# Optimization experiments

Hardware: AMD Instinct MI355X
Metric: run time of the kernel (lower is better)

## Reference

```python
import jax, jax.numpy as jnp
import numpy as np

SEQ_LEN, INPUT_DIM, HIDDEN_DIM, NUM_CLASSES, BATCH = 512, 256, 1024, 128, 256


def setup_inputs() -> dict:
    key = jax.random.key(0)
    ks = jax.random.split(key, 12)
    sx = np.sqrt(2.0 / INPUT_DIM).astype(np.float32)
    sh = np.sqrt(2.0 / HIDDEN_DIM).astype(np.float32)
    inp = {
        "x": jax.random.randint(ks[0], (BATCH, SEQ_LEN, 1), 0, NUM_CLASSES, dtype=jnp.int32),
        "emb": jax.random.normal(ks[1], (NUM_CLASSES, INPUT_DIM), jnp.float32),
        "Wcx": jax.random.normal(ks[2], (HIDDEN_DIM, INPUT_DIM), jnp.float32) * sx,
        "bc": jnp.zeros((HIDDEN_DIM,), jnp.float32),
        "Wix": jax.random.normal(ks[3], (HIDDEN_DIM, INPUT_DIM), jnp.float32) * sx,
        "Wih": jax.random.normal(ks[4], (HIDDEN_DIM, HIDDEN_DIM), jnp.float32) * sh,
        "bi": jnp.zeros((HIDDEN_DIM,), jnp.float32),
        "Wfx": jax.random.normal(ks[5], (HIDDEN_DIM, INPUT_DIM), jnp.float32) * sx,
        "Wfh": jax.random.normal(ks[6], (HIDDEN_DIM, HIDDEN_DIM), jnp.float32) * sh,
        "bf": jnp.zeros((HIDDEN_DIM,), jnp.float32),
        "Wox": jax.random.normal(ks[7], (HIDDEN_DIM, INPUT_DIM), jnp.float32) * sx,
        "Woh": jax.random.normal(ks[8], (HIDDEN_DIM, HIDDEN_DIM), jnp.float32) * sh,
        "bo": jnp.zeros((HIDDEN_DIM,), jnp.float32),
        "Wph": jax.random.normal(ks[9], (NUM_CLASSES, HIDDEN_DIM), jnp.float32) * sh,
        "bp": jnp.zeros((NUM_CLASSES,), jnp.float32),
    }
    return inp


def reference(x, emb, Wcx, bc, Wix, Wih, bi, Wfx, Wfh, bf, Wox, Woh, bo, Wph, bp):
    B = x.shape[0]
    H = Wfh.shape[0]
    xt = emb[x[:, :, 0]]                       # [B, S, I] embedded inputs
    # Precompute the input-to-gate projections (parallel over time; identical math)
    xf = jnp.einsum("bsi,hi->sbh", xt, Wfx)    # [S, B, H]
    xi = jnp.einsum("bsi,hi->sbh", xt, Wix)
    xo = jnp.einsum("bsi,hi->sbh", xt, Wox)
    xc = jnp.einsum("bsi,hi->sbh", xt, Wcx)

    def step(carry, inputs):
        c, h = carry
        xf_t, xi_t, xo_t, xc_t = inputs
        # peephole gates read cell state c, not h
        f = jax.nn.sigmoid(xf_t + c @ Wfh.T + bf)
        i = jax.nn.sigmoid(xi_t + c @ Wih.T + bi)
        o = jax.nn.sigmoid(xo_t + c @ Woh.T + bo)
        c_new = jax.nn.sigmoid(xc_t + bc) * i + c * f
        h_new = jnp.tanh(c_new) * o
        return (c_new, h_new), None

    c0 = jnp.zeros((B, H), xt.dtype)
    h0 = jnp.zeros((B, H), xt.dtype)
    (c_T, h_T), _ = jax.lax.scan(step, (c0, h0), (xf, xi, xo, xc))
    p = h_T @ Wph.T + bp                       # [B, num_classes]
    return jax.nn.log_softmax(p, axis=1)
```

## Files before the change

kernel.cpp:

```cpp
#include <hip/hip_runtime.h>

#define SEQ  512
#define IDIM 256
#define H    1024
#define NC   128
#define B    256
#define NBLK 256

typedef __attribute__((ext_vector_type(8))) short bh8;
typedef __attribute__((ext_vector_type(4))) float f4;
typedef __attribute__((ext_vector_type(4))) int i4;

__device__ __forceinline__ float sigf(float x) { return 1.0f / (1.0f + __expf(-x)); }

__device__ __forceinline__ unsigned short bf16r(float v) {
    unsigned u = __builtin_bit_cast(unsigned, v);
    u += 0x7fffu + ((u >> 16) & 1u);
    return (unsigned short)(u >> 16);
}

__global__ __launch_bounds__(256) void tables_kernel(
    const float* __restrict__ emb,
    const float* __restrict__ Wcx, const float* __restrict__ bc,
    const float* __restrict__ Wix, const float* __restrict__ bi,
    const float* __restrict__ Wfx, const float* __restrict__ bf,
    const float* __restrict__ Wox, const float* __restrict__ bo,
    float* __restrict__ FF, float* __restrict__ II,
    float* __restrict__ OO, float* __restrict__ G)
{
    const int k = blockIdx.x;
    const int h = blockIdx.y * 256 + threadIdx.x;
    __shared__ float e[IDIM];
    e[threadIdx.x] = emb[k * IDIM + threadIdx.x];
    __syncthreads();
    const float4* e4  = (const float4*)e;
    const float4* wf4 = (const float4*)(Wfx + (size_t)h * IDIM);
    const float4* wi4 = (const float4*)(Wix + (size_t)h * IDIM);
    const float4* wo4 = (const float4*)(Wox + (size_t)h * IDIM);
    const float4* wc4 = (const float4*)(Wcx + (size_t)h * IDIM);
    float aF = 0.f, aI = 0.f, aO = 0.f, aC = 0.f;
#pragma unroll 4
    for (int i = 0; i < IDIM / 4; i++) {
        float4 ev = e4[i];
        float4 a = wf4[i]; aF += ev.x * a.x + ev.y * a.y + ev.z * a.z + ev.w * a.w;
        float4 b = wi4[i]; aI += ev.x * b.x + ev.y * b.y + ev.z * b.z + ev.w * b.w;
        float4 c = wo4[i]; aO += ev.x * c.x + ev.y * c.y + ev.z * c.z + ev.w * c.w;
        float4 d = wc4[i]; aC += ev.x * d.x + ev.y * d.y + ev.z * d.z + ev.w * d.w;
    }
    const int o = k * H + h;
    FF[o] = aF + bf[h];
    II[o] = aI + bi[h];
    OO[o] = aO + bo[h];
    G[o]  = sigf(aC + bc[h]);
}

__global__ __launch_bounds__(256) void swz_kernel(const float* __restrict__ W,
                                                  unsigned short* __restrict__ D)
{
    int g = blockIdx.x * 256 + threadIdx.x;
    int h  = g >> 7;
    int kc = (g & 127) << 3;
    const float4* s = (const float4*)(W + (size_t)h * H + kc);
    float4 a = s[0], b = s[1];
    unsigned short tmp[8] = { bf16r(a.x), bf16r(a.y), bf16r(a.z), bf16r(a.w),
                              bf16r(b.x), bf16r(b.y), bf16r(b.z), bf16r(b.w) };
    int nb = h >> 4, kb = kc >> 5, quad = (kc >> 3) & 3;
    int lane = (h & 15) + (quad << 4);
    bh8 v;
#pragma unroll
    for (int j = 0; j < 8; j++) v[j] = (short)tmp[j];
    *(bh8*)(D + (size_t)((nb * 32 + kb) * 512 + lane * 8)) = v;
}

__global__ __launch_bounds__(256, 1) void persist_kernel(
    const unsigned short* __restrict__ Wf, const unsigned short* __restrict__ Wi,
    const unsigned short* __restrict__ Wo,
    const float* __restrict__ FF, const float* __restrict__ II,
    const float* __restrict__ OO, const float* __restrict__ G,
    const int* __restrict__ x,
    unsigned short* c16a, unsigned short* c16b,
    float* __restrict__ hb, int* flags)
{
    const int blk = blockIdx.x;
    const int rt = blk >> 4;
    const int nt = blk & 15;
    const int tid  = threadIdx.x;
    const int wave = tid >> 6;
    const int lane = tid & 63;
    const int l15 = lane & 15, quad = lane >> 4;

    __shared__ unsigned short cs[16 * 1024];

    const int row0 = rt * 16;
    const int abase = l15 * 1024;
    const int asw = l15 & 7;
    const int hcol = nt * 64 + wave * 16 + l15;
    const int nb = nt * 4 + wave;

    const unsigned short* wfp = Wf + (size_t)nb * 32 * 512 + (size_t)lane * 8;
    const unsigned short* wip = Wi + (size_t)nb * 32 * 512 + (size_t)lane * 8;
    const unsigned short* wop = Wo + (size_t)nb * 32 * 512 + (size_t)lane * 8;

    bh8 wf_r[32], wi_r[32];
#pragma unroll
    for (int kt = 0; kt < 32; kt++) {
        wf_r[kt] = *(const bh8*)(wfp + (size_t)kt * 512);
        wi_r[kt] = *(const bh8*)(wip + (size_t)kt * 512);
    }

    float cn_keep[4] = {0.f, 0.f, 0.f, 0.f};
    int* const myflag = flags + rt * 64 + nt * 4 + wave;
    const int* const pf = flags + rt * 64 + lane;

    for (int s = 0; s < SEQ; s++) {
        const unsigned short* cur16 = (s & 1) ? c16b : c16a;
        unsigned short*       nxt16 = (s & 1) ? c16a : c16b;

        float ffv[4], iiv[4], ggv[4];
#pragma unroll
        for (int r = 0; r < 4; r++) {
            int b = row0 + quad * 4 + r;
            int tok = x[b * SEQ + s];
            ffv[r] = FF[tok * H + hcol];
            iiv[r] = II[tok * H + hcol];
            ggv[r] = G[tok * H + hcol];
        }

        f4 accF = {0.f, 0.f, 0.f, 0.f}, accI = {0.f, 0.f, 0.f, 0.f};
        if (s > 0) {
            {
                int guard = 0;
                for (;;) {
                    int fv;
                    asm volatile("global_load_dword %0, %1, off sc0 sc1\n\ts_waitcnt vmcnt(0)"
                                 : "=v"(fv) : "v"(pf) : "memory");
                    if (__all(fv >= s)) break;
                    if (++guard > (1 << 20)) break;
                }
            }
            i4 tmp[8];
#pragma unroll
            for (int i = 0; i < 8; i++) {
                int chunk = i * 256 + tid;
                int row = chunk >> 7, g = chunk & 127;
                const i4* p = (const i4*)(cur16 + (size_t)(row0 + row) * H + g * 8);
                asm volatile("global_load_dwordx4 %0, %1, off sc0 sc1"
                             : "=v"(tmp[i]) : "v"(p));
            }
            asm volatile("s_waitcnt vmcnt(0)" ::: "memory");
#pragma unroll
            for (int i = 0; i < 8; i++) {
                int chunk = i * 256 + tid;
                int row = chunk >> 7, g = chunk & 127;
                *(i4*)(cs + row * 1024 + ((g ^ (row & 7)) << 3)) = tmp[i];
            }
            __syncthreads();
#pragma unroll
            for (int kt = 0; kt < 32; kt++) {
                bh8 a = *(const bh8*)(cs + abase + (((kt * 4 + quad) ^ asw) << 3));
                accF = __builtin_amdgcn_mfma_f32_16x16x32_bf16(a, wf_r[kt], accF, 0, 0, 0);
                accI = __builtin_amdgcn_mfma_f32_16x16x32_bf16(a, wi_r[kt], accI, 0, 0, 0);
            }
        }

#pragma unroll
        for (int r = 0; r < 4; r++) {
            float f = sigf(ffv[r] + accF[r]);
            float i = sigf(iiv[r] + accI[r]);
            float cn = ggv[r] * i + cn_keep[r] * f;
            cn_keep[r] = cn;
            int b = row0 + quad * 4 + r;
            unsigned us = bf16r(cn);
            unsigned ot = (unsigned)__shfl_xor((int)us, 1);
            if (s < SEQ - 1 && (lane & 1) == 0) {
                unsigned dw = us | (ot << 16);
                unsigned* p = (unsigned*)(nxt16 + (size_t)b * H + hcol);
                asm volatile("global_atomic_swap %0, %1, off sc1"
                             :: "v"(p), "v"(dw) : "memory");
            }
        }

        if (s < SEQ - 1) {
            asm volatile("s_waitcnt vmcnt(0)" ::: "memory");
            if (lane == 0) {
                int v = s + 1;
                asm volatile("global_atomic_swap %0, %1, off sc1"
                             :: "v"(myflag), "v"(v) : "memory");
            }
        }
    }

    f4 accO = {0.f, 0.f, 0.f, 0.f};
#pragma unroll 4
    for (int kt = 0; kt < 32; kt++) {
        bh8 a  = *(const bh8*)(cs + abase + (((kt * 4 + quad) ^ asw) << 3));
        bh8 bo = *(const bh8*)(wop + (size_t)kt * 512);
        accO = __builtin_amdgcn_mfma_f32_16x16x32_bf16(a, bo, accO, 0, 0, 0);
    }
#pragma unroll
    for (int r = 0; r < 4; r++) {
        int b = row0 + quad * 4 + r;
        int tok = x[b * SEQ + (SEQ - 1)];
        float o = sigf(OO[tok * H + hcol] + accO[r]);
        hb[(size_t)b * H + hcol] = tanhf(cn_keep[r]) * o;
    }
}

__global__ __launch_bounds__(128) void out_kernel(
    const float* __restrict__ hbuf, const float* __restrict__ Wph,
    const float* __restrict__ bp, float* __restrict__ out)
{
    const int b = blockIdx.x;
    const int j = threadIdx.x;
    __shared__ float hs[H];
    for (int t = j; t < H; t += 128) hs[t] = hbuf[(size_t)b * H + t];
    __syncthreads();
    const float4* w4 = (const float4*)(Wph + (size_t)j * H);
    const float4* h4 = (const float4*)hs;
    float acc = bp[j];
#pragma unroll 4
    for (int k = 0; k < H / 4; k++) {
        float4 a = w4[k], v = h4[k];
        acc += a.x * v.x + a.y * v.y + a.z * v.z + a.w * v.w;
    }
    __shared__ float red[128];
    red[j] = acc; __syncthreads();
    for (int off = 64; off > 0; off >>= 1) { if (j < off) red[j] = fmaxf(red[j], red[j + off]); __syncthreads(); }
    float m = red[0]; __syncthreads();
    red[j] = __expf(acc - m); __syncthreads();
    for (int off = 64; off > 0; off >>= 1) { if (j < off) red[j] += red[j + off]; __syncthreads(); }
    float lse = m + __logf(red[0]);
    out[(size_t)b * NC + j] = acc - lse;
}

extern "C" void kernel_launch(void* const* d_in, const int* in_sizes, int n_in,
                              void* d_out, int out_size, void* d_ws, size_t ws_size,
                              hipStream_t stream)
{
    const int*   x   = (const int*)d_in[0];
    const float* emb = (const float*)d_in[1];
    const float* Wcx = (const float*)d_in[2];
    const float* bc  = (const float*)d_in[3];
    const float* Wix = (const float*)d_in[4];
    const float* Wih = (const float*)d_in[5];
    const float* bi  = (const float*)d_in[6];
    const float* Wfx = (const float*)d_in[7];
    const float* Wfh = (const float*)d_in[8];
    const float* bf  = (const float*)d_in[9];
    const float* Wox = (const float*)d_in[10];
    const float* Woh = (const float*)d_in[11];
    const float* bo  = (const float*)d_in[12];
    const float* Wph = (const float*)d_in[13];
    const float* bp  = (const float*)d_in[14];
    float* out = (float*)d_out;

    char* wsb = (char*)d_ws;
    float* FF = (float*)(wsb + 0);
    float* II = (float*)(wsb + (512 << 10));
    float* OO = (float*)(wsb + (1024 << 10));
    float* G  = (float*)(wsb + (1536 << 10));
    float* hb = (float*)(wsb + (2048 << 10));
    int*   flags = (int*)(wsb + (3072 << 10));
    unsigned short* Wf_sw = (unsigned short*)(wsb + (4096 << 10));
    unsigned short* Wi_sw = (unsigned short*)(wsb + (6144 << 10));
    unsigned short* Wo_sw = (unsigned short*)(wsb + (8192 << 10));
    unsigned short* c16a  = (unsigned short*)(wsb + (10240 << 10));
    unsigned short* c16b  = (unsigned short*)(wsb + (10752 << 10));

    hipMemsetAsync(flags, 0, 4096, stream);

    tables_kernel<<<dim3(NC, 4), 256, 0, stream>>>(emb, Wcx, bc, Wix, bi, Wfx, bf, Wox, bo,
                                                   FF, II, OO, G);
    swz_kernel<<<512, 256, 0, stream>>>(Wfh, Wf_sw);
    swz_kernel<<<512, 256, 0, stream>>>(Wih, Wi_sw);
    swz_kernel<<<512, 256, 0, stream>>>(Woh, Wo_sw);

    persist_kernel<<<NBLK, 256, 0, stream>>>(Wf_sw, Wi_sw, Wo_sw, FF, II, OO, G, x,
                                             c16a, c16b, hb, flags);

    out_kernel<<<B, 128, 0, stream>>>(hb, Wph, bp, out);
}
```

Before: 2.340 ms.

## Replace per-wave flag barrier with step-tagged cell-state words for dataflow sync

Each cell-state element is now stored as a 32-bit word whose high half carries the step tag and low half the bf16 value. Consumers poll the data itself until every tag reaches the current step, re-polling only the chunks that are not yet ready. This removes the separate flag write, the vmcnt wait before it, and the flag-polling round trip, so data and readiness arrive together. The cost is that cell-state traffic and global loads double, and readers must unpack the tagged words with perm instructions.

```diff
diff --git a/kernel.cpp b/kernel.cpp
--- a/kernel.cpp
+++ b/kernel.cpp
@@ -18,6 +18,8 @@
     u += 0x7fffu + ((u >> 16) & 1u);
     return (unsigned short)(u >> 16);
 }
+
+__device__ __forceinline__ unsigned umin2(unsigned a, unsigned b) { return a < b ? a : b; }
 
 __global__ __launch_bounds__(256) void tables_kernel(
     const float* __restrict__ emb,
@@ -78,8 +80,8 @@
     const float* __restrict__ FF, const float* __restrict__ II,
     const float* __restrict__ OO, const float* __restrict__ G,
     const int* __restrict__ x,
-    unsigned short* c16a, unsigned short* c16b,
-    float* __restrict__ hb, int* flags)
+    unsigned* c32a, unsigned* c32b,
+    float* __restrict__ hb)
 {
     const int blk = blockIdx.x;
     const int rt = blk >> 4;
@@ -109,12 +111,10 @@
     }
 
     float cn_keep[4] = {0.f, 0.f, 0.f, 0.f};
-    int* const myflag = flags + rt * 64 + nt * 4 + wave;
-    const int* const pf = flags + rt * 64 + lane;
 
     for (int s = 0; s < SEQ; s++) {
-        const unsigned short* cur16 = (s & 1) ? c16b : c16a;
-        unsigned short*       nxt16 = (s & 1) ? c16a : c16b;
+        const unsigned* curb = (s & 1) ? c32b : c32a;
+        unsigned*       nxtb = (s & 1) ? c32a : c32b;
 
         float ffv[4], iiv[4], ggv[4];
 #pragma unroll
@@ -128,31 +128,52 @@
 
         f4 accF = {0.f, 0.f, 0.f, 0.f}, accI = {0.f, 0.f, 0.f, 0.f};
         if (s > 0) {
-            {
-                int guard = 0;
-                for (;;) {
-                    int fv;
-                    asm volatile("global_load_dword %0, %1, off sc0 sc1\n\ts_waitcnt vmcnt(0)"
-                                 : "=v"(fv) : "v"(pf) : "memory");
-                    if (__all(fv >= s)) break;
-                    if (++guard > (1 << 20)) break;
+            const unsigned thrs = ((unsigned)s) << 16;
+            i4 ta[8], tb[8];
+            bool done[8];
+#pragma unroll
+            for (int i = 0; i < 8; i++) done[i] = false;
+            int guard = 0;
+            for (;;) {
+#pragma unroll
+                for (int i = 0; i < 8; i++) {
+                    if (!done[i]) {
+                        int chunk = i * 256 + tid;
+                        int row = chunk >> 7, g = chunk & 127;
+                        const i4* p = (const i4*)(curb + (size_t)(row0 + row) * 1024 + g * 8);
+                        asm volatile("global_load_dwordx4 %0, %1, off sc0 sc1"
+                                     : "=v"(ta[i]) : "v"(p));
+                        asm volatile("global_load_dwordx4 %0, %1, off sc0 sc1"
+                                     : "=v"(tb[i]) : "v"(p + 1));
+                    }
                 }
-            }
-            i4 tmp[8];
+                asm volatile("s_waitcnt vmcnt(0)" ::: "memory");
+                bool all = true;
+#pragma unroll
+                for (int i = 0; i < 8; i++) {
+                    if (!done[i]) {
+                        unsigned m = umin2(
+                            umin2(umin2((unsigned)ta[i].x, (unsigned)ta[i].y),
+                                  umin2((unsigned)ta[i].z, (unsigned)ta[i].w)),
+                            umin2(umin2((unsigned)tb[i].x, (unsigned)tb[i].y),
+                                  umin2((unsigned)tb[i].z, (unsigned)tb[i].w)));
+                        done[i] = (m >= thrs);
+                    }
+                    all = all && done[i];
+                }
+                if (all) break;
+                if (++guard > (1 << 16)) break;
+            }
 #pragma unroll
             for (int i = 0; i < 8; i++) {
                 int chunk = i * 256 + tid;
                 int row = chunk >> 7, g = chunk & 127;
-                const i4* p = (const i4*)(cur16 + (size_t)(row0 + row) * H + g * 8);
-                asm volatile("global_load_dwordx4 %0, %1, off sc0 sc1"
-                             : "=v"(tmp[i]) : "v"(p));
-            }
-            asm volatile("s_waitcnt vmcnt(0)" ::: "memory");
-#pragma unroll
-            for (int i = 0; i < 8; i++) {
-                int chunk = i * 256 + tid;
-                int row = chunk >> 7, g = chunk & 127;
-                *(i4*)(cs + row * 1024 + ((g ^ (row & 7)) << 3)) = tmp[i];
+                i4 pv;
+                pv.x = (int)__builtin_amdgcn_perm((unsigned)ta[i].y, (unsigned)ta[i].x, 0x05040100u);
+                pv.y = (int)__builtin_amdgcn_perm((unsigned)ta[i].w, (unsigned)ta[i].z, 0x05040100u);
+                pv.z = (int)__builtin_amdgcn_perm((unsigned)tb[i].y, (unsigned)tb[i].x, 0x05040100u);
+                pv.w = (int)__builtin_amdgcn_perm((unsigned)tb[i].w, (unsigned)tb[i].z, 0x05040100u);
+                *(i4*)(cs + row * 1024 + ((g ^ (row & 7)) << 3)) = pv;
             }
             __syncthreads();
 #pragma unroll
@@ -163,29 +184,19 @@
             }
         }
 
+        const unsigned tagw = ((unsigned)(s + 1)) << 16;
 #pragma unroll
         for (int r = 0; r < 4; r++) {
             float f = sigf(ffv[r] + accF[r]);
             float i = sigf(iiv[r] + accI[r]);
             float cn = ggv[r] * i + cn_keep[r] * f;
             cn_keep[r] = cn;
-            int b = row0 + quad * 4 + r;
-            unsigned us = bf16r(cn);
-            unsigned ot = (unsigned)__shfl_xor((int)us, 1);
-            if (s < SEQ - 1 && (lane & 1) == 0) {
-                unsigned dw = us | (ot << 16);
-                unsigned* p = (unsigned*)(nxt16 + (size_t)b * H + hcol);
+            if (s < SEQ - 1) {
+                int b = row0 + quad * 4 + r;
+                unsigned dw = tagw | (unsigned)bf16r(cn);
+                unsigned* p = nxtb + (size_t)b * 1024 + hcol;
                 asm volatile("global_atomic_swap %0, %1, off sc1"
                              :: "v"(p), "v"(dw) : "memory");
-            }
-        }
-
-        if (s < SEQ - 1) {
-            asm volatile("s_waitcnt vmcnt(0)" ::: "memory");
-            if (lane == 0) {
-                int v = s + 1;
-                asm volatile("global_atomic_swap %0, %1, off sc1"
-                             :: "v"(myflag), "v"(v) : "memory");
             }
         }
     }
@@ -260,14 +271,13 @@
     float* OO = (float*)(wsb + (1024 << 10));
     float* G  = (float*)(wsb + (1536 << 10));
     float* hb = (float*)(wsb + (2048 << 10));
-    int*   flags = (int*)(wsb + (3072 << 10));
-    unsigned short* Wf_sw = (unsigned short*)(wsb + (4096 << 10));
-    unsigned short* Wi_sw = (unsigned short*)(wsb + (6144 << 10));
-    unsigned short* Wo_sw = (unsigned short*)(wsb + (8192 << 10));
-    unsigned short* c16a  = (unsigned short*)(wsb + (10240 << 10));
-    unsigned short* c16b  = (unsigned short*)(wsb + (10752 << 10));
-
-    hipMemsetAsync(flags, 0, 4096, stream);
+    unsigned* c32a = (unsigned*)(wsb + (3072 << 10));
+    unsigned* c32b = (unsigned*)(wsb + (4096 << 10));
+    unsigned short* Wf_sw = (unsigned short*)(wsb + (5120 << 10));
+    unsigned short* Wi_sw = (unsigned short*)(wsb + (7168 << 10));
+    unsigned short* Wo_sw = (unsigned short*)(wsb + (9216 << 10));
+
+    hipMemsetAsync(c32a, 0, 2 << 20, stream);
 
     tables_kernel<<<dim3(NC, 4), 256, 0, stream>>>(emb, Wcx, bc, Wix, bi, Wfx, bf, Wox, bo,
                                                    FF, II, OO, G);
@@ -276,7 +286,7 @@
     swz_kernel<<<512, 256, 0, stream>>>(Woh, Wo_sw);
 
     persist_kernel<<<NBLK, 256, 0, stream>>>(Wf_sw, Wi_sw, Wo_sw, FF, II, OO, G, x,
-                                             c16a, c16b, hb, flags);
+                                             c32a, c32b, hb);
 
     out_kernel<<<B, 128, 0, stream>>>(hb, Wph, bp, out);
 }
```

After: 3.090 ms. +32.0%, slower.

## Ping-pong two batch row groups per block to overlap sync latency with compute

Applied to the files above, without the earlier changes.

Halves the persistent grid so each block handles two 16-row batch groups (A and B) that share the same register-resident weight tiles. The step loop is software-pipelined: while group A's flag poll and global loads of the previous cell state are in flight, the epilogue and flag publish for group B run, and the reverse. The aim is to hide the cross-block flag-wait and global-load latency of the recurrence behind useful work. In exchange each block does twice the MFMA and epilogue work per step, uses twice the LDS, and only half as many CUs participate.

```diff
diff --git a/kernel.cpp b/kernel.cpp
--- a/kernel.cpp
+++ b/kernel.cpp
@@ -5,7 +5,7 @@
 #define H    1024
 #define NC   128
 #define B    256
-#define NBLK 256
+#define NBLK 128
 
 typedef __attribute__((ext_vector_type(8))) short bh8;
 typedef __attribute__((ext_vector_type(4))) float f4;
@@ -72,6 +72,56 @@
     *(bh8*)(D + (size_t)((nb * 32 + kb) * 512 + lane * 8)) = v;
 }
 
+#define ATOMSW(p_, v_) asm volatile("global_atomic_swap %0, %1, off sc1" :: "v"(p_), "v"(v_) : "memory")
+#define POLL(pf_, thr_)                                                                     \
+    { int guard_ = 0;                                                                       \
+      for (;;) { int fv_;                                                                   \
+        asm volatile("global_load_dword %0, %1, off sc0 sc1\n\ts_waitcnt vmcnt(0)"          \
+                     : "=v"(fv_) : "v"(pf_) : "memory");                                    \
+        if (__all(fv_ >= (thr_))) break;                                                    \
+        if (++guard_ > (1 << 20)) break; } }
+#define STAGE_ISSUE(tmp_, cur_, row0_)                                                      \
+    _Pragma("unroll")                                                                       \
+    for (int i_ = 0; i_ < 8; i_++) {                                                        \
+        int chunk_ = i_ * 256 + tid;                                                        \
+        int row_ = chunk_ >> 7, g_ = chunk_ & 127;                                          \
+        const i4* p_ = (const i4*)((cur_) + (size_t)((row0_) + row_) * H + g_ * 8);         \
+        asm volatile("global_load_dwordx4 %0, %1, off sc0 sc1" : "=v"(tmp_[i_]) : "v"(p_)); }
+#define LDS_WRITE(cs_, tmp_)                                                                \
+    _Pragma("unroll")                                                                       \
+    for (int i_ = 0; i_ < 8; i_++) {                                                        \
+        int chunk_ = i_ * 256 + tid;                                                        \
+        int row_ = chunk_ >> 7, g_ = chunk_ & 127;                                          \
+        *(i4*)((cs_) + row_ * 1024 + ((g_ ^ (row_ & 7)) << 3)) = tmp_[i_]; }
+#define LOAD_TABLES(row0_, s_, ffv_, iiv_, ggv_)                                            \
+    _Pragma("unroll")                                                                       \
+    for (int r_ = 0; r_ < 4; r_++) {                                                        \
+        int b_ = (row0_) + quad * 4 + r_;                                                   \
+        int tok_ = x[b_ * SEQ + (s_)];                                                      \
+        ffv_[r_] = FF[tok_ * H + hcol];                                                     \
+        iiv_[r_] = II[tok_ * H + hcol];                                                     \
+        ggv_[r_] = G[tok_ * H + hcol]; }
+#define MFMA32(cs_, accF_, accI_)                                                           \
+    _Pragma("unroll")                                                                       \
+    for (int kt_ = 0; kt_ < 32; kt_++) {                                                    \
+        bh8 a_ = *(const bh8*)((cs_) + abase + (((kt_ * 4 + quad) ^ asw) << 3));            \
+        accF_ = __builtin_amdgcn_mfma_f32_16x16x32_bf16(a_, wf_r[kt_], accF_, 0, 0, 0);     \
+        accI_ = __builtin_amdgcn_mfma_f32_16x16x32_bf16(a_, wi_r[kt_], accI_, 0, 0, 0); }
+#define EPILOGUE(ffv_, iiv_, ggv_, accF_, accI_, cn_, row0_, nxt_, do_store_)               \
+    _Pragma("unroll")                                                                       \
+    for (int r_ = 0; r_ < 4; r_++) {                                                        \
+        float f_ = sigf(ffv_[r_] + accF_[r_]);                                              \
+        float i_ = sigf(iiv_[r_] + accI_[r_]);                                              \
+        float cn2_ = ggv_[r_] * i_ + cn_[r_] * f_;                                          \
+        cn_[r_] = cn2_;                                                                     \
+        int b_ = (row0_) + quad * 4 + r_;                                                   \
+        unsigned us_ = bf16r(cn2_);                                                         \
+        unsigned ot_ = (unsigned)__shfl_xor((int)us_, 1);                                   \
+        if ((do_store_) && (lane & 1) == 0) {                                               \
+            unsigned dw_ = us_ | (ot_ << 16);                                               \
+            unsigned* p_ = (unsigned*)((nxt_) + (size_t)b_ * H + hcol);                     \
+            ATOMSW(p_, dw_); } }
+
 __global__ __launch_bounds__(256, 1) void persist_kernel(
     const unsigned short* __restrict__ Wf, const unsigned short* __restrict__ Wi,
     const unsigned short* __restrict__ Wo,
@@ -82,16 +132,18 @@
     float* __restrict__ hb, int* flags)
 {
     const int blk = blockIdx.x;
-    const int rt = blk >> 4;
-    const int nt = blk & 15;
+    const int set = blk >> 4;
+    const int nt  = blk & 15;
+    const int gA = set * 2, gB = set * 2 + 1;
+    const int rowA0 = gA * 16, rowB0 = gB * 16;
     const int tid  = threadIdx.x;
     const int wave = tid >> 6;
     const int lane = tid & 63;
     const int l15 = lane & 15, quad = lane >> 4;
 
-    __shared__ unsigned short cs[16 * 1024];
-
-    const int row0 = rt * 16;
+    __shared__ unsigned short csA[16 * 1024];
+    __shared__ unsigned short csB[16 * 1024];
+
     const int abase = l15 * 1024;
     const int asw = l15 & 7;
     const int hcol = nt * 64 + wave * 16 + l15;
@@ -108,101 +160,70 @@
         wi_r[kt] = *(const bh8*)(wip + (size_t)kt * 512);
     }
 
-    float cn_keep[4] = {0.f, 0.f, 0.f, 0.f};
-    int* const myflag = flags + rt * 64 + nt * 4 + wave;
-    const int* const pf = flags + rt * 64 + lane;
-
-    for (int s = 0; s < SEQ; s++) {
+    int* const mfA = flags + gA * 64 + nt * 4 + wave;
+    const int* const pfA = flags + gA * 64 + lane;
+    int* const mfB = flags + gB * 64 + nt * 4 + wave;
+    const int* const pfB = flags + gB * 64 + lane;
+
+    float cnA[4] = {0.f, 0.f, 0.f, 0.f}, cnB[4] = {0.f, 0.f, 0.f, 0.f};
+    f4 accFA = {0,0,0,0}, accIA = {0,0,0,0};
+    f4 accFB = {0,0,0,0}, accIB = {0,0,0,0};
+    float ffvA[4], iivA[4], ggvA[4], ffvB[4], iivB[4], ggvB[4];
+
+    LOAD_TABLES(rowA0, 0, ffvA, iivA, ggvA);
+    LOAD_TABLES(rowB0, 0, ffvB, iivB, ggvB);
+    EPILOGUE(ffvA, iivA, ggvA, accFA, accIA, cnA, rowA0, c16b, 1);
+    asm volatile("s_waitcnt vmcnt(0)" ::: "memory");
+    if (lane == 0) { int v = 1; ATOMSW(mfA, v); }
+
+    for (int s = 1; s < SEQ; s++) {
         const unsigned short* cur16 = (s & 1) ? c16b : c16a;
         unsigned short*       nxt16 = (s & 1) ? c16a : c16b;
-
-        float ffv[4], iiv[4], ggv[4];
-#pragma unroll
-        for (int r = 0; r < 4; r++) {
-            int b = row0 + quad * 4 + r;
-            int tok = x[b * SEQ + s];
-            ffv[r] = FF[tok * H + hcol];
-            iiv[r] = II[tok * H + hcol];
-            ggv[r] = G[tok * H + hcol];
-        }
-
-        f4 accF = {0.f, 0.f, 0.f, 0.f}, accI = {0.f, 0.f, 0.f, 0.f};
-        if (s > 0) {
-            {
-                int guard = 0;
-                for (;;) {
-                    int fv;
-                    asm volatile("global_load_dword %0, %1, off sc0 sc1\n\ts_waitcnt vmcnt(0)"
-                                 : "=v"(fv) : "v"(pf) : "memory");
-                    if (__all(fv >= s)) break;
-                    if (++guard > (1 << 20)) break;
-                }
-            }
-            i4 tmp[8];
-#pragma unroll
-            for (int i = 0; i < 8; i++) {
-                int chunk = i * 256 + tid;
-                int row = chunk >> 7, g = chunk & 127;
-                const i4* p = (const i4*)(cur16 + (size_t)(row0 + row) * H + g * 8);
-                asm volatile("global_load_dwordx4 %0, %1, off sc0 sc1"
-                             : "=v"(tmp[i]) : "v"(p));
-            }
-            asm volatile("s_waitcnt vmcnt(0)" ::: "memory");
-#pragma unroll
-            for (int i = 0; i < 8; i++) {
-                int chunk = i * 256 + tid;
-                int row = chunk >> 7, g = chunk & 127;
-                *(i4*)(cs + row * 1024 + ((g ^ (row & 7)) << 3)) = tmp[i];
-            }
-            __syncthreads();
-#pragma unroll
-            for (int kt = 0; kt < 32; kt++) {
-                bh8 a = *(const bh8*)(cs + abase + (((kt * 4 + quad) ^ asw) << 3));
-                accF = __builtin_amdgcn_mfma_f32_16x16x32_bf16(a, wf_r[kt], accF, 0, 0, 0);
-                accI = __builtin_amdgcn_mfma_f32_16x16x32_bf16(a, wi_r[kt], accI, 0, 0, 0);
-            }
-        }
-
-#pragma unroll
-        for (int r = 0; r < 4; r++) {
-            float f = sigf(ffv[r] + accF[r]);
-            float i = sigf(iiv[r] + accI[r]);
-            float cn = ggv[r] * i + cn_keep[r] * f;
-            cn_keep[r] = cn;
-            int b = row0 + quad * 4 + r;
-            unsigned us = bf16r(cn);
-            unsigned ot = (unsigned)__shfl_xor((int)us, 1);
-            if (s < SEQ - 1 && (lane & 1) == 0) {
-                unsigned dw = us | (ot << 16);
-                unsigned* p = (unsigned*)(nxt16 + (size_t)b * H + hcol);
-                asm volatile("global_atomic_swap %0, %1, off sc1"
-                             :: "v"(p), "v"(dw) : "memory");
-            }
-        }
-
-        if (s < SEQ - 1) {
-            asm volatile("s_waitcnt vmcnt(0)" ::: "memory");
-            if (lane == 0) {
-                int v = s + 1;
-                asm volatile("global_atomic_swap %0, %1, off sc1"
-                             :: "v"(myflag), "v"(v) : "memory");
-            }
-        }
-    }
-
-    f4 accO = {0.f, 0.f, 0.f, 0.f};
+        POLL(pfA, s);
+        i4 tmpA[8];
+        STAGE_ISSUE(tmpA, cur16, rowA0);
+        LOAD_TABLES(rowA0, s, ffvA, iivA, ggvA);
+        EPILOGUE(ffvB, iivB, ggvB, accFB, accIB, cnB, rowB0, cur16, 1);
+        asm volatile("s_waitcnt vmcnt(0)" ::: "memory");
+        if (lane == 0) { int v = s; ATOMSW(mfB, v); }
+        LDS_WRITE(csA, tmpA);
+        __syncthreads();
+        accFA = (f4){0,0,0,0}; accIA = (f4){0,0,0,0};
+        MFMA32(csA, accFA, accIA);
+        POLL(pfB, s);
+        i4 tmpB[8];
+        STAGE_ISSUE(tmpB, cur16, rowB0);
+        LOAD_TABLES(rowB0, s, ffvB, iivB, ggvB);
+        EPILOGUE(ffvA, iivA, ggvA, accFA, accIA, cnA, rowA0, nxt16, (s < SEQ - 1));
+        asm volatile("s_waitcnt vmcnt(0)" ::: "memory");
+        if (s < SEQ - 1 && lane == 0) { int v = s + 1; ATOMSW(mfA, v); }
+        LDS_WRITE(csB, tmpB);
+        __syncthreads();
+        accFB = (f4){0,0,0,0}; accIB = (f4){0,0,0,0};
+        MFMA32(csB, accFB, accIB);
+    }
+
+    EPILOGUE(ffvB, iivB, ggvB, accFB, accIB, cnB, rowB0, c16a, 0);
+
+    f4 accOA = {0,0,0,0}, accOB = {0,0,0,0};
 #pragma unroll 4
     for (int kt = 0; kt < 32; kt++) {
-        bh8 a  = *(const bh8*)(cs + abase + (((kt * 4 + quad) ^ asw) << 3));
         bh8 bo = *(const bh8*)(wop + (size_t)kt * 512);
-        accO = __builtin_amdgcn_mfma_f32_16x16x32_bf16(a, bo, accO, 0, 0, 0);
+        bh8 aA = *(const bh8*)(csA + abase + (((kt * 4 + quad) ^ asw) << 3));
+        bh8 aB = *(const bh8*)(csB + abase + (((kt * 4 + quad) ^ asw) << 3));
+        accOA = __builtin_amdgcn_mfma_f32_16x16x32_bf16(aA, bo, accOA, 0, 0, 0);
+        accOB = __builtin_amdgcn_mfma_f32_16x16x32_bf16(aB, bo, accOB, 0, 0, 0);
     }
 #pragma unroll
     for (int r = 0; r < 4; r++) {
-        int b = row0 + quad * 4 + r;
-        int tok = x[b * SEQ + (SEQ - 1)];
-        float o = sigf(OO[tok * H + hcol] + accO[r]);
-        hb[(size_t)b * H + hcol] = tanhf(cn_keep[r]) * o;
+        int bA = rowA0 + quad * 4 + r;
+        int tokA = x[bA * SEQ + (SEQ - 1)];
+        float oA = sigf(OO[tokA * H + hcol] + accOA[r]);
+        hb[(size_t)bA * H + hcol] = tanhf(cnA[r]) * oA;
+        int bB = rowB0 + quad * 4 + r;
+        int tokB = x[bB * SEQ + (SEQ - 1)];
+        float oB = sigf(OO[tokB * H + hcol] + accOB[r]);
+        hb[(size_t)bB * H + hcol] = tanhf(cnB[r]) * oB;
     }
 }
 
@@ -267,7 +288,7 @@
     unsigned short* c16a  = (unsigned short*)(wsb + (10240 << 10));
     unsigned short* c16b  = (unsigned short*)(wsb + (10752 << 10));
 
-    hipMemsetAsync(flags, 0, 4096, stream);
+    (void)hipMemsetAsync(flags, 0, 4096, stream);
 
     tables_kernel<<<dim3(NC, 4), 256, 0, stream>>>(emb, Wcx, bc, Wix, bi, Wfx, bf, Wox, bo,
                                                    FF, II, OO, G);
```

After: 5.595 ms. 2.39x slower.

## Use per-block flags and fetch ready producer slices eagerly in recurrent loop

Applied to the files above, without the earlier changes.

Replaces the per-wave readiness flags with one flag per block, published after a block-wide barrier. Consumers no longer wait until every producer is ready before loading. They ballot the flags and issue loads for each producer's 64-column slice as soon as that slice is ready, starting from the next neighbour to spread the traffic. Cell-state stores are widened to 64-bit atomic swaps. This overlaps loading with waiting and cuts flag traffic, at the cost of an extra __syncthreads per step and more, smaller loads.

```diff
diff --git a/kernel.cpp b/kernel.cpp
--- a/kernel.cpp
+++ b/kernel.cpp
@@ -10,6 +10,7 @@
 typedef __attribute__((ext_vector_type(8))) short bh8;
 typedef __attribute__((ext_vector_type(4))) float f4;
 typedef __attribute__((ext_vector_type(4))) int i4;
+typedef __attribute__((ext_vector_type(2))) int i2;
 
 __device__ __forceinline__ float sigf(float x) { return 1.0f / (1.0f + __expf(-x)); }
 
@@ -97,6 +98,9 @@
     const int hcol = nt * 64 + wave * 16 + l15;
     const int nb = nt * 4 + wave;
 
+    const int prow = tid >> 4;
+    const int pc8  = tid & 15;
+
     const unsigned short* wfp = Wf + (size_t)nb * 32 * 512 + (size_t)lane * 8;
     const unsigned short* wip = Wi + (size_t)nb * 32 * 512 + (size_t)lane * 8;
     const unsigned short* wop = Wo + (size_t)nb * 32 * 512 + (size_t)lane * 8;
@@ -109,8 +113,8 @@
     }
 
     float cn_keep[4] = {0.f, 0.f, 0.f, 0.f};
-    int* const myflag = flags + rt * 64 + nt * 4 + wave;
-    const int* const pf = flags + rt * 64 + lane;
+    int* const myflag = flags + rt * 16 + nt;
+    const int* const pf = flags + rt * 16 + (lane & 15);
 
     for (int s = 0; s < SEQ; s++) {
         const unsigned short* cur16 = (s & 1) ? c16b : c16a;
@@ -128,31 +132,33 @@
 
         f4 accF = {0.f, 0.f, 0.f, 0.f}, accI = {0.f, 0.f, 0.f, 0.f};
         if (s > 0) {
-            {
-                int guard = 0;
-                for (;;) {
-                    int fv;
-                    asm volatile("global_load_dword %0, %1, off sc0 sc1\n\ts_waitcnt vmcnt(0)"
-                                 : "=v"(fv) : "v"(pf) : "memory");
-                    if (__all(fv >= s)) break;
-                    if (++guard > (1 << 20)) break;
+            i2 tmp[16];
+            unsigned done = 0;
+            int guard = 0;
+            while (done != 0xffffu) {
+                int fv;
+                asm volatile("global_load_dword %0, %1, off sc0 sc1\n\ts_waitcnt vmcnt(0)"
+                             : "=v"(fv) : "v"(pf) : "memory");
+                unsigned rdy = (unsigned)__ballot(fv >= s) & 0xffffu & ~done;
+#pragma unroll
+                for (int p = 0; p < 16; p++) {
+                    int q = (nt + 1 + p) & 15;
+                    if ((rdy >> q) & 1u) {
+                        const i2* src = (const i2*)(cur16 + (size_t)(row0 + prow) * H
+                                                    + q * 64 + pc8 * 4);
+                        asm volatile("global_load_dwordx2 %0, %1, off sc0 sc1"
+                                     : "=v"(tmp[p]) : "v"(src));
+                    }
                 }
-            }
-            i4 tmp[8];
-#pragma unroll
-            for (int i = 0; i < 8; i++) {
-                int chunk = i * 256 + tid;
-                int row = chunk >> 7, g = chunk & 127;
-                const i4* p = (const i4*)(cur16 + (size_t)(row0 + row) * H + g * 8);
-                asm volatile("global_load_dwordx4 %0, %1, off sc0 sc1"
-                             : "=v"(tmp[i]) : "v"(p));
+                done |= rdy;
+                if (++guard > (1 << 20)) break;
             }
             asm volatile("s_waitcnt vmcnt(0)" ::: "memory");
 #pragma unroll
-            for (int i = 0; i < 8; i++) {
-                int chunk = i * 256 + tid;
-                int row = chunk >> 7, g = chunk & 127;
-                *(i4*)(cs + row * 1024 + ((g ^ (row & 7)) << 3)) = tmp[i];
+            for (int p = 0; p < 16; p++) {
+                int q = (nt + 1 + p) & 15;
+                int g = q * 8 + (pc8 >> 1);
+                *(i2*)(cs + prow * 1024 + ((g ^ (prow & 7)) << 3) + (pc8 & 1) * 4) = tmp[p];
             }
             __syncthreads();
 #pragma unroll
@@ -172,17 +178,21 @@
             int b = row0 + quad * 4 + r;
             unsigned us = bf16r(cn);
             unsigned ot = (unsigned)__shfl_xor((int)us, 1);
-            if (s < SEQ - 1 && (lane & 1) == 0) {
-                unsigned dw = us | (ot << 16);
-                unsigned* p = (unsigned*)(nxt16 + (size_t)b * H + hcol);
-                asm volatile("global_atomic_swap %0, %1, off sc1"
-                             :: "v"(p), "v"(dw) : "memory");
+            unsigned dw = us | (ot << 16);
+            unsigned dwhi = (unsigned)__shfl_xor((int)dw, 2);
+            if (s < SEQ - 1 && (lane & 3) == 0) {
+                unsigned long long qw = (unsigned long long)dw
+                                      | ((unsigned long long)dwhi << 32);
+                unsigned long long* p = (unsigned long long*)(nxt16 + (size_t)b * H + hcol);
+                asm volatile("global_atomic_swap_x2 %0, %1, off sc1"
+                             :: "v"(p), "v"(qw) : "memory");
             }
         }
 
         if (s < SEQ - 1) {
             asm volatile("s_waitcnt vmcnt(0)" ::: "memory");
-            if (lane == 0) {
+            __syncthreads();
+            if (tid == 0) {
                 int v = s + 1;
                 asm volatile("global_atomic_swap %0, %1, off sc1"
                              :: "v"(myflag), "v"(v) : "memory");
@@ -267,7 +277,7 @@
     unsigned short* c16a  = (unsigned short*)(wsb + (10240 << 10));
     unsigned short* c16b  = (unsigned short*)(wsb + (10752 << 10));
 
-    hipMemsetAsync(flags, 0, 4096, stream);
+    (void)hipMemsetAsync(flags, 0, 1024, stream);
 
     tables_kernel<<<dim3(NC, 4), 256, 0, stream>>>(emb, Wcx, bc, Wix, bi, Wfx, bf, Wox, bo,
                                                    FF, II, OO, G);
```

Measured after the change: 2.701 ms. 1.15x slower.
